# Performance work log

Hardware: AMD Instinct MI355X
Metric: run time of the kernel (lower is better)

The kernel has to match this reference:

```python
import jax, jax.numpy as jnp
import numpy as np
import math

SCALE = 64.0
MARGIN = 0.5
EPS = 1e-07
COS_M = math.cos(MARGIN)
SIN_M = math.sin(MARGIN)
THRESHOLD = math.cos(math.pi - MARGIN)
MM = math.sin(math.pi - MARGIN) * MARGIN

N, D, C = 512, 512, 100000


def setup_inputs() -> dict:
    key = jax.random.key(0)
    k1, k2, k3 = jax.random.split(key, 3)
    x = jax.random.normal(k1, (N, D), dtype=jnp.float32)
    weight = jax.random.normal(k2, (C, D), dtype=jnp.float32)
    t = jnp.zeros((1,), dtype=jnp.float32)
    target = jax.random.randint(k3, (N,), 0, C, dtype=jnp.int64)
    return {"x": x, "weight": weight, "t": t, "target": target}


def reference(x, weight, t, target):
    # normalized linear -> cosine similarities [N, C]
    xn = x / jnp.linalg.norm(x, axis=1, keepdims=True)
    wn = weight / jnp.linalg.norm(weight, axis=1, keepdims=True)
    cos_theta = jnp.clip(jnp.einsum('nd,cd->nc', xn, wn), -1.0 + EPS, 1.0 - EPS)

    rows = jnp.arange(cos_theta.shape[0])
    target_logit = cos_theta[rows, target][:, None]            # [N, 1]
    sin_theta = jnp.sqrt(1.0 - target_logit * target_logit)
    cos_theta_m = target_logit * COS_M - sin_theta * SIN_M      # cos(theta + m)

    mask = cos_theta > cos_theta_m                              # hard examples
    final_target_logit = jnp.where(target_logit > THRESHOLD,
                                   cos_theta_m,
                                   target_logit - MM)

    # EMA buffer update (no-grad in torch)
    t_new = jax.lax.stop_gradient(target_logit.mean() * 0.01 + 0.99 * t)  # [1]

    # hard-example re-weighting: cos * (t + cos) where mask
    cos_theta = jnp.where(mask, cos_theta * (t_new[0] + cos_theta), cos_theta)
    # scatter margin-adjusted target logit into target column
    cos_theta = cos_theta.at[rows, target].set(final_target_logit[:, 0])

    logits = cos_theta * SCALE
    # cross entropy (mean)
    logp = jax.nn.log_softmax(logits, axis=-1)
    loss = -jnp.mean(logp[rows, target])
    return loss
```

## Files before the change

kernel.cpp:

```cpp
#include <hip/hip_runtime.h>
#include <hip/hip_bf16.h>
#include <stdint.h>

#define N_ROWS 512
#define D_DIM  512
#define C_CLS  100000

#define SCALE_F    64.0f
#define EPS_F      1e-7f
#define COS_M_F    0.8775825618903728f
#define SIN_M_F    0.4794255386042030f
#define THRESH_F  -0.8775825618903728f
#define MM_F       0.2397127693021015f
#define FIXMAX_F   65.0f

#define NC  64
#define NG2 1564

#define XN8_OFF    0
#define TL_OFF     (XN8_OFF + 512*512)
#define CTM_OFF    (TL_OFF + 2048)
#define FTL_OFF    (CTM_OFF + 2048)
#define TNEW_OFF   (FTL_OFF + 2048)
#define XNORM_OFF  (TNEW_OFF + 256)
#define PSUM_OFF   (XNORM_OFF + 2048)
#define LOSSI_OFF  (PSUM_OFF + NG2*512*4)

typedef __attribute__((ext_vector_type(4))) float f32x4;

#define GLOAD_LDS16(gp, lp) \
    __builtin_amdgcn_global_load_lds((const __attribute__((address_space(1))) void*)(gp), \
                                     (__attribute__((address_space(3))) void*)(lp), 16, 0, 0)

#if defined(__has_builtin)
#if __has_builtin(__builtin_amdgcn_cvt_pk_fp8_f32)
#define HAVE_CVT_FP8 1
#endif
#endif

__device__ inline unsigned char f2e4m3(float f) {
    union { float f; unsigned u; } a; a.f = f;
    unsigned s = (a.u >> 24) & 0x80u;
    float af = fabsf(f);
    if (af < 0.015625f) {
        int q = (int)(af * 512.0f + 0.5f);
        return (unsigned char)(s | (unsigned)q);
    }
    unsigned x = a.u & 0x7FFFFFFFu;
    unsigned r = x + 0x000FFFFFu + ((x >> 20) & 1u);
    int ec = (int)(r >> 23) - 127 + 7;
    unsigned m = (r >> 20) & 7u;
    if (ec > 15 || (ec == 15 && m == 7u)) return (unsigned char)(s | 0x7Eu);
    return (unsigned char)(s | ((unsigned)ec << 3) | m);
}

__device__ inline unsigned pack4_fp8(float f0, float f1, float f2, float f3) {
#ifdef HAVE_CVT_FP8
    int q = __builtin_amdgcn_cvt_pk_fp8_f32(f0, f1, 0, false);
    q     = __builtin_amdgcn_cvt_pk_fp8_f32(f2, f3, q, true);
    return (unsigned)q;
#else
    union { unsigned char b[4]; unsigned u; } u;
    u.b[0]=f2e4m3(f0); u.b[1]=f2e4m3(f1); u.b[2]=f2e4m3(f2); u.b[3]=f2e4m3(f3);
    return u.u;
#endif
}

__device__ inline uint2 pack8_fp8(float f0, float f1, float f2, float f3,
                                  float f4, float f5, float f6, float f7) {
    uint2 r;
    r.x = pack4_fp8(f0, f1, f2, f3);
    r.y = pack4_fp8(f4, f5, f6, f7);
    return r;
}

__device__ inline float wave_sum64(float v) {
    #pragma unroll
    for (int m = 1; m < 64; m <<= 1) v += __shfl_xor(v, m);
    return v;
}

__global__ void k_xnorm_fp8(const float* __restrict__ x,
                            unsigned char* __restrict__ xn8,
                            float* __restrict__ xnorm) {
    int row = blockIdx.x;
    int lane = threadIdx.x;
    const float* xr = x + row * D_DIM + lane * 8;
    float4 v0 = *(const float4*)(xr);
    float4 v1 = *(const float4*)(xr + 4);
    float s = v0.x*v0.x + v0.y*v0.y + v0.z*v0.z + v0.w*v0.w
            + v1.x*v1.x + v1.y*v1.y + v1.z*v1.z + v1.w*v1.w;
    s = wave_sum64(s);
    float nrm = sqrtf(s);
    if (lane == 0) xnorm[row] = nrm;
    float inv = 1.0f / nrm;
    uint2 q = pack8_fp8(v0.x*inv, v0.y*inv, v0.z*inv, v0.w*inv,
                        v1.x*inv, v1.y*inv, v1.z*inv, v1.w*inv);
    *(uint2*)(xn8 + row * D_DIM + lane * 8) = q;
}

__global__ void k_tlogit(const float* __restrict__ x, const float* __restrict__ w,
                         const float* __restrict__ xnorm,
                         const int* __restrict__ target,
                         float* __restrict__ tl, float* __restrict__ ctm,
                         float* __restrict__ ftl) {
    int row = blockIdx.x;
    int lane = threadIdx.x;
    int tgt = target[row];
    const float* xr = x + row * D_DIM + lane * 8;
    const float* wr = w + (size_t)tgt * D_DIM + lane * 8;
    float4 a0 = *(const float4*)(xr),     a1 = *(const float4*)(xr + 4);
    float4 b0 = *(const float4*)(wr),     b1 = *(const float4*)(wr + 4);
    float s = a0.x*b0.x + a0.y*b0.y + a0.z*b0.z + a0.w*b0.w
            + a1.x*b1.x + a1.y*b1.y + a1.z*b1.z + a1.w*b1.w;
    float q = b0.x*b0.x + b0.y*b0.y + b0.z*b0.z + b0.w*b0.w
            + b1.x*b1.x + b1.y*b1.y + b1.z*b1.z + b1.w*b1.w;
    s = wave_sum64(s);
    q = wave_sum64(q);
    if (lane == 0) {
        float c = s / (xnorm[row] * sqrtf(q));
        c = fminf(fmaxf(c, -1.0f + EPS_F), 1.0f - EPS_F);
        float sn = sqrtf(fmaxf(1.0f - c * c, 0.0f));
        float cm = c * COS_M_F - sn * SIN_M_F;
        tl[row]  = c;
        ctm[row] = cm;
        ftl[row] = (c > THRESH_F) ? cm : (c - MM_F);
    }
}

__global__ void k_tnew(const float* __restrict__ tl, const float* __restrict__ t,
                       float* __restrict__ tnew) {
    __shared__ float s[512];
    int tid = threadIdx.x;
    s[tid] = tl[tid];
    __syncthreads();
    for (int off = 256; off > 0; off >>= 1) {
        if (tid < off) s[tid] += s[tid + off];
        __syncthreads();
    }
    if (tid == 0) tnew[0] = (s[0] / 512.0f) * 0.01f + 0.99f * t[0];
}

__global__ __launch_bounds__(512, 4) void k_fused(
        const unsigned char* __restrict__ xn8,
        const float* __restrict__ w,
        const int* __restrict__ target,
        const float* __restrict__ ctm,
        const float* __restrict__ ftl,
        const float* __restrict__ tnew,
        float* __restrict__ psum) {
    __shared__ unsigned char As[2][512 * 32];
    __shared__ unsigned char Bs[2][64 * 32];
    __shared__ float invS[64];
    __shared__ int   tgt_s[512];
    __shared__ float ctm_s[512];
    __shared__ float ftl_s[512];

    int bx = blockIdx.x;
    int cb = bx * NC;
    int tid = threadIdx.x;
    int lane = tid & 63, wid = tid >> 6;
    int fr = lane & 15, rgrp = lane >> 4;
    int wrow = wid * 64;

    tgt_s[tid] = target[tid];
    ctm_s[tid] = ctm[tid];
    ftl_s[tid] = ftl[tid];

    int brow  = tid >> 3;
    int bslot = tid & 7;
    int bclass = cb + brow;
    bool brvalid = (bclass < C_CLS);
    const float* bsrc = w + (size_t)(brvalid ? bclass : 0) * D_DIM + bslot * 4;

    float sumsq = 0.0f;

    #define STAGE_A(kk, buf)                                                  \
        do {                                                                  \
            _Pragma("unroll")                                                 \
            for (int c = 0; c < 2; ++c) {                                     \
                int lo = c * 8192 + wid * 1024;             \
                int o  = lo + lane * 16;                                      \
                int row = o >> 5, b = o & 31;                                 \
                GLOAD_LDS16(xn8 + (size_t)row * 512 + (kk) * 32 + b,          \
                            (char*)As[buf] + lo);                             \
            }                                                                 \
        } while (0)

    #define WRITE_B(vv, buf)                                                  \
        do {                                                                  \
            sumsq += vv.x*vv.x + vv.y*vv.y + vv.z*vv.z + vv.w*vv.w;           \
            *(unsigned*)(&Bs[buf][brow * 32 + bslot * 4]) =                   \
                pack4_fp8(vv.x, vv.y, vv.z, vv.w);                            \
        } while (0)

    float4 rv_next = *(const float4*)(bsrc + 1 * 32);
    float4 rv_far  = *(const float4*)(bsrc + 2 * 32);
    {
        float4 v0 = *(const float4*)(bsrc);
        WRITE_B(v0, 0);
    }
    STAGE_A(0, 0);
    __syncthreads();

    float tn = tnew[0];

    f32x4 acc[4][4];
    #pragma unroll
    for (int m = 0; m < 4; m++)
        #pragma unroll
        for (int j = 0; j < 4; j++)
            acc[m][j] = (f32x4){0.f, 0.f, 0.f, 0.f};

    union LL { uint2 u; long long ll; };

    #pragma unroll
    for (int kk = 0; kk < 16; ++kk) {
        int cur = kk & 1;
        if (kk < 15) {
            WRITE_B(rv_next, cur ^ 1);
            rv_next = rv_far;
            if (kk < 13)
                rv_far = *(const float4*)(bsrc + (kk + 3) * 32);
            STAGE_A(kk + 1, cur ^ 1);
        }
        uint2 af[4], bf[4];
        #pragma unroll
        for (int m = 0; m < 4; m++)
            af[m] = *(const uint2*)(&As[cur][(wrow + m * 16 + fr) * 32 + rgrp * 8]);
        #pragma unroll
        for (int j = 0; j < 4; j++)
            bf[j] = *(const uint2*)(&Bs[cur][(j * 16 + fr) * 32 + rgrp * 8]);
        __builtin_amdgcn_s_setprio(1);
        #pragma unroll
        for (int m = 0; m < 4; m++)
            #pragma unroll
            for (int j = 0; j < 4; j++) {
                LL a, b;
                a.u = af[m];
                b.u = bf[j];
                acc[m][j] = __builtin_amdgcn_mfma_f32_16x16x32_fp8_fp8(
                                a.ll, b.ll, acc[m][j], 0, 0, 0);
            }
        __builtin_amdgcn_s_setprio(0);
        __syncthreads();
    }
    #undef STAGE_A
    #undef WRITE_B

    float s2 = sumsq;
    s2 += __shfl_xor(s2, 1);
    s2 += __shfl_xor(s2, 2);
    s2 += __shfl_xor(s2, 4);
    if (bslot == 0) invS[brow] = rsqrtf(s2);
    __syncthreads();

    float inv[4];
    bool cvalid[4];
    #pragma unroll
    for (int j = 0; j < 4; j++) {
        inv[j] = invS[j * 16 + fr];
        cvalid[j] = (cb + j * 16 + fr) < C_CLS;
    }
    #pragma unroll
    for (int m = 0; m < 4; m++) {
        #pragma unroll
        for (int reg = 0; reg < 4; reg++) {
            int rl = wrow + m * 16 + rgrp * 4 + reg;
            int tr = tgt_s[rl];
            float cm = ctm_s[rl];
            float ft = ftl_s[rl];
            float sm = 0.0f;
            #pragma unroll
            for (int j = 0; j < 4; j++) {
                int col = cb + j * 16 + fr;
                float c = acc[m][j][reg] * inv[j];
                c = fminf(fmaxf(c, -1.0f + EPS_F), 1.0f - EPS_F);
                float v = (c > cm) ? c * (tn + c) : c;
                v *= SCALE_F;
                v = (col == tr) ? ft * SCALE_F : v;
                v = cvalid[j] ? v : -3.0e38f;
                sm += __expf(v - FIXMAX_F);
            }
            #pragma unroll
            for (int msk = 1; msk < 16; msk <<= 1) sm += __shfl_xor(sm, msk);
            if (fr == 0) psum[(size_t)bx * 512 + rl] = sm;
        }
    }
}

__global__ void k_rowlse_fix(const float* __restrict__ psum,
                             const float* __restrict__ ftl,
                             float* __restrict__ lossi) {
    int row = blockIdx.x, tid = threadIdx.x;
    float S = 0.0f;
    for (int nb = tid; nb < NG2; nb += 256) S += psum[(size_t)nb * 512 + row];
    __shared__ float sS[256];
    sS[tid] = S;
    __syncthreads();
    for (int off = 128; off > 0; off >>= 1) {
        if (tid < off) sS[tid] += sS[tid + off];
        __syncthreads();
    }
    if (tid == 0) lossi[row] = logf(sS[0]) + FIXMAX_F - SCALE_F * ftl[row];
}

__global__ void k_final(const float* __restrict__ lossi, float* __restrict__ out) {
    __shared__ float s[512];
    int tid = threadIdx.x;
    s[tid] = lossi[tid];
    __syncthreads();
    for (int off = 256; off > 0; off >>= 1) {
        if (tid < off) s[tid] += s[tid + off];
        __syncthreads();
    }
    if (tid == 0) out[0] = s[0] / 512.0f;
}

extern "C" void kernel_launch(void* const* d_in, const int* in_sizes, int n_in,
                              void* d_out, int out_size, void* d_ws, size_t ws_size,
                              hipStream_t stream) {
    const float* x      = (const float*)d_in[0];
    const float* w      = (const float*)d_in[1];
    const float* t      = (const float*)d_in[2];
    const int*   target = (const int*)d_in[3];

    char* ws = (char*)d_ws;
    unsigned char* xn8  = (unsigned char*)(ws + XN8_OFF);
    float* tl    = (float*)(ws + TL_OFF);
    float* ctm   = (float*)(ws + CTM_OFF);
    float* ftl   = (float*)(ws + FTL_OFF);
    float* tnew  = (float*)(ws + TNEW_OFF);
    float* xnorm = (float*)(ws + XNORM_OFF);
    float* psum  = (float*)(ws + PSUM_OFF);
    float* lossi = (float*)(ws + LOSSI_OFF);
    float* out   = (float*)d_out;

    k_xnorm_fp8<<<dim3(N_ROWS), dim3(64), 0, stream>>>(x, xn8, xnorm);
    k_tlogit<<<dim3(N_ROWS), dim3(64), 0, stream>>>(x, w, xnorm, target, tl, ctm, ftl);
    k_tnew<<<dim3(1), dim3(512), 0, stream>>>(tl, t, tnew);
    k_fused<<<dim3(NG2), dim3(512), 0, stream>>>(xn8, w, target, ctm, ftl, tnew, psum);
    k_rowlse_fix<<<dim3(N_ROWS), dim3(256), 0, stream>>>(psum, ftl, lossi);
    k_final<<<dim3(1), dim3(512), 0, stream>>>(lossi, out);
}
```

Before: 123.8 us.

## Load A fragments directly into registers and use 1024-thread blocks in fused GEMM

The fused GEMM kernel no longer stages the normalized x matrix through LDS. Each wave keeps its A fragments in registers with a three-deep prefetch from global memory, and blocks grow to 1024 threads with 32 rows per wave. The B tile gets a padded LDS stride to reduce bank conflicts, and the two prep kernels merge into one, dropping the xnorm buffer. This removes LDS traffic and capacity pressure for A, but depends on the 256KB xn8 matrix staying cache-resident and raises register and barrier pressure from the larger blocks.

```diff
diff --git a/kernel.cpp b/kernel.cpp
--- a/kernel.cpp
+++ b/kernel.cpp
@@ -22,15 +22,10 @@
 #define CTM_OFF    (TL_OFF + 2048)
 #define FTL_OFF    (CTM_OFF + 2048)
 #define TNEW_OFF   (FTL_OFF + 2048)
-#define XNORM_OFF  (TNEW_OFF + 256)
-#define PSUM_OFF   (XNORM_OFF + 2048)
+#define PSUM_OFF   (TNEW_OFF + 256)
 #define LOSSI_OFF  (PSUM_OFF + NG2*512*4)
 
 typedef __attribute__((ext_vector_type(4))) float f32x4;
-
-#define GLOAD_LDS16(gp, lp) \
-    __builtin_amdgcn_global_load_lds((const __attribute__((address_space(1))) void*)(gp), \
-                                     (__attribute__((address_space(3))) void*)(lp), 16, 0, 0)
 
 #if defined(__has_builtin)
 #if __has_builtin(__builtin_amdgcn_cvt_pk_fp8_f32)
@@ -66,12 +61,13 @@
 #endif
 }
 
-__device__ inline uint2 pack8_fp8(float f0, float f1, float f2, float f3,
-                                  float f4, float f5, float f6, float f7) {
-    uint2 r;
-    r.x = pack4_fp8(f0, f1, f2, f3);
-    r.y = pack4_fp8(f4, f5, f6, f7);
-    return r;
+__device__ inline unsigned short pack2_fp8(float f0, float f1) {
+#ifdef HAVE_CVT_FP8
+    int q = __builtin_amdgcn_cvt_pk_fp8_f32(f0, f1, 0, false);
+    return (unsigned short)(q & 0xFFFF);
+#else
+    return (unsigned short)(f2e4m3(f0) | ((unsigned short)f2e4m3(f1) << 8));
+#endif
 }
 
 __device__ inline float wave_sum64(float v) {
@@ -80,45 +76,37 @@
     return v;
 }
 
-__global__ void k_xnorm_fp8(const float* __restrict__ x,
-                            unsigned char* __restrict__ xn8,
-                            float* __restrict__ xnorm) {
+__global__ void k_prep(const float* __restrict__ x, const float* __restrict__ w,
+                       const int* __restrict__ target,
+                       unsigned char* __restrict__ xn8,
+                       float* __restrict__ tl, float* __restrict__ ctm,
+                       float* __restrict__ ftl) {
     int row = blockIdx.x;
     int lane = threadIdx.x;
     const float* xr = x + row * D_DIM + lane * 8;
     float4 v0 = *(const float4*)(xr);
     float4 v1 = *(const float4*)(xr + 4);
-    float s = v0.x*v0.x + v0.y*v0.y + v0.z*v0.z + v0.w*v0.w
-            + v1.x*v1.x + v1.y*v1.y + v1.z*v1.z + v1.w*v1.w;
-    s = wave_sum64(s);
-    float nrm = sqrtf(s);
-    if (lane == 0) xnorm[row] = nrm;
+    float sx = v0.x*v0.x + v0.y*v0.y + v0.z*v0.z + v0.w*v0.w
+             + v1.x*v1.x + v1.y*v1.y + v1.z*v1.z + v1.w*v1.w;
+    sx = wave_sum64(sx);
+    float nrm = sqrtf(sx);
     float inv = 1.0f / nrm;
-    uint2 q = pack8_fp8(v0.x*inv, v0.y*inv, v0.z*inv, v0.w*inv,
-                        v1.x*inv, v1.y*inv, v1.z*inv, v1.w*inv);
-    *(uint2*)(xn8 + row * D_DIM + lane * 8) = q;
-}
-
-__global__ void k_tlogit(const float* __restrict__ x, const float* __restrict__ w,
-                         const float* __restrict__ xnorm,
-                         const int* __restrict__ target,
-                         float* __restrict__ tl, float* __restrict__ ctm,
-                         float* __restrict__ ftl) {
-    int row = blockIdx.x;
-    int lane = threadIdx.x;
+    uint2 q8;
+    q8.x = pack4_fp8(v0.x*inv, v0.y*inv, v0.z*inv, v0.w*inv);
+    q8.y = pack4_fp8(v1.x*inv, v1.y*inv, v1.z*inv, v1.w*inv);
+    *(uint2*)(xn8 + row * D_DIM + lane * 8) = q8;
+
     int tgt = target[row];
-    const float* xr = x + row * D_DIM + lane * 8;
     const float* wr = w + (size_t)tgt * D_DIM + lane * 8;
-    float4 a0 = *(const float4*)(xr),     a1 = *(const float4*)(xr + 4);
-    float4 b0 = *(const float4*)(wr),     b1 = *(const float4*)(wr + 4);
-    float s = a0.x*b0.x + a0.y*b0.y + a0.z*b0.z + a0.w*b0.w
-            + a1.x*b1.x + a1.y*b1.y + a1.z*b1.z + a1.w*b1.w;
+    float4 b0 = *(const float4*)(wr), b1 = *(const float4*)(wr + 4);
+    float s = v0.x*b0.x + v0.y*b0.y + v0.z*b0.z + v0.w*b0.w
+            + v1.x*b1.x + v1.y*b1.y + v1.z*b1.z + v1.w*b1.w;
     float q = b0.x*b0.x + b0.y*b0.y + b0.z*b0.z + b0.w*b0.w
             + b1.x*b1.x + b1.y*b1.y + b1.z*b1.z + b1.w*b1.w;
     s = wave_sum64(s);
     q = wave_sum64(q);
     if (lane == 0) {
-        float c = s / (xnorm[row] * sqrtf(q));
+        float c = s / (nrm * sqrtf(q));
         c = fminf(fmaxf(c, -1.0f + EPS_F), 1.0f - EPS_F);
         float sn = sqrtf(fmaxf(1.0f - c * c, 0.0f));
         float cm = c * COS_M_F - sn * SIN_M_F;
@@ -141,7 +129,7 @@
     if (tid == 0) tnew[0] = (s[0] / 512.0f) * 0.01f + 0.99f * t[0];
 }
 
-__global__ __launch_bounds__(512, 4) void k_fused(
+__global__ __launch_bounds__(1024, 4) void k_fused(
         const unsigned char* __restrict__ xn8,
         const float* __restrict__ w,
         const int* __restrict__ target,
@@ -149,8 +137,7 @@
         const float* __restrict__ ftl,
         const float* __restrict__ tnew,
         float* __restrict__ psum) {
-    __shared__ unsigned char As[2][512 * 32];
-    __shared__ unsigned char Bs[2][64 * 32];
+    __shared__ unsigned char Bs[2][64 * 40];
     __shared__ float invS[64];
     __shared__ int   tgt_s[512];
     __shared__ float ctm_s[512];
@@ -161,53 +148,45 @@
     int tid = threadIdx.x;
     int lane = tid & 63, wid = tid >> 6;
     int fr = lane & 15, rgrp = lane >> 4;
-    int wrow = wid * 64;
-
-    tgt_s[tid] = target[tid];
-    ctm_s[tid] = ctm[tid];
-    ftl_s[tid] = ftl[tid];
-
-    int brow  = tid >> 3;
-    int bslot = tid & 7;
+    int wrow = wid * 32;
+
+    if (tid < 512) {
+        tgt_s[tid] = target[tid];
+        ctm_s[tid] = ctm[tid];
+        ftl_s[tid] = ftl[tid];
+    }
+    float tn = tnew[0];
+
+    int brow  = tid >> 4;
+    int bslot = tid & 15;
     int bclass = cb + brow;
-    bool brvalid = (bclass < C_CLS);
-    const float* bsrc = w + (size_t)(brvalid ? bclass : 0) * D_DIM + bslot * 4;
-
+    const float* bsrc = w + (size_t)(bclass < C_CLS ? bclass : 0) * D_DIM + bslot * 2;
+    int bwaddr = brow * 40 + bslot * 2;
     float sumsq = 0.0f;
 
-    #define STAGE_A(kk, buf)                                                  \
-        do {                                                                  \
-            _Pragma("unroll")                                                 \
-            for (int c = 0; c < 2; ++c) {                                     \
-                int lo = c * 8192 + wid * 1024;             \
-                int o  = lo + lane * 16;                                      \
-                int row = o >> 5, b = o & 31;                                 \
-                GLOAD_LDS16(xn8 + (size_t)row * 512 + (kk) * 32 + b,          \
-                            (char*)As[buf] + lo);                             \
-            }                                                                 \
-        } while (0)
-
-    #define WRITE_B(vv, buf)                                                  \
-        do {                                                                  \
-            sumsq += vv.x*vv.x + vv.y*vv.y + vv.z*vv.z + vv.w*vv.w;           \
-            *(unsigned*)(&Bs[buf][brow * 32 + bslot * 4]) =                   \
-                pack4_fp8(vv.x, vv.y, vv.z, vv.w);                            \
-        } while (0)
-
-    float4 rv_next = *(const float4*)(bsrc + 1 * 32);
-    float4 rv_far  = *(const float4*)(bsrc + 2 * 32);
+    const unsigned char* asrc0 = xn8 + (size_t)(wrow + fr) * D_DIM + rgrp * 8;
+    const unsigned char* asrc1 = xn8 + (size_t)(wrow + 16 + fr) * D_DIM + rgrp * 8;
+
     {
-        float4 v0 = *(const float4*)(bsrc);
-        WRITE_B(v0, 0);
-    }
-    STAGE_A(0, 0);
-    __syncthreads();
-
-    float tn = tnew[0];
-
-    f32x4 acc[4][4];
-    #pragma unroll
-    for (int m = 0; m < 4; m++)
+        float2 v0 = *(const float2*)(bsrc);
+        sumsq += v0.x*v0.x + v0.y*v0.y;
+        *(unsigned short*)(&Bs[0][bwaddr]) = pack2_fp8(v0.x, v0.y);
+    }
+    float2 rvN = *(const float2*)(bsrc + 32);
+    float2 rvF = *(const float2*)(bsrc + 64);
+    uint2 aP0 = *(const uint2*)(asrc0);
+    uint2 aP1 = *(const uint2*)(asrc1);
+    uint2 aQ0 = *(const uint2*)(asrc0 + 32);
+    uint2 aQ1 = *(const uint2*)(asrc1 + 32);
+    uint2 aR0 = *(const uint2*)(asrc0 + 64);
+    uint2 aR1 = *(const uint2*)(asrc1 + 64);
+    asm volatile("s_waitcnt lgkmcnt(0)" ::: "memory");
+    __builtin_amdgcn_s_barrier();
+    __builtin_amdgcn_sched_barrier(0);
+
+    f32x4 acc[2][4];
+    #pragma unroll
+    for (int m = 0; m < 2; m++)
         #pragma unroll
         for (int j = 0; j < 4; j++)
             acc[m][j] = (f32x4){0.f, 0.f, 0.f, 0.f};
@@ -217,41 +196,42 @@
     #pragma unroll
     for (int kk = 0; kk < 16; ++kk) {
         int cur = kk & 1;
-        if (kk < 15) {
-            WRITE_B(rv_next, cur ^ 1);
-            rv_next = rv_far;
-            if (kk < 13)
-                rv_far = *(const float4*)(bsrc + (kk + 3) * 32);
-            STAGE_A(kk + 1, cur ^ 1);
-        }
-        uint2 af[4], bf[4];
-        #pragma unroll
-        for (int m = 0; m < 4; m++)
-            af[m] = *(const uint2*)(&As[cur][(wrow + m * 16 + fr) * 32 + rgrp * 8]);
+        uint2 bf[4];
         #pragma unroll
         for (int j = 0; j < 4; j++)
-            bf[j] = *(const uint2*)(&Bs[cur][(j * 16 + fr) * 32 + rgrp * 8]);
+            bf[j] = *(const uint2*)(&Bs[cur][(j * 16 + fr) * 40 + rgrp * 8]);
         __builtin_amdgcn_s_setprio(1);
         #pragma unroll
-        for (int m = 0; m < 4; m++)
-            #pragma unroll
-            for (int j = 0; j < 4; j++) {
-                LL a, b;
-                a.u = af[m];
-                b.u = bf[j];
-                acc[m][j] = __builtin_amdgcn_mfma_f32_16x16x32_fp8_fp8(
-                                a.ll, b.ll, acc[m][j], 0, 0, 0);
+        for (int j = 0; j < 4; j++) {
+            LL a0, a1, b;
+            a0.u = aP0; a1.u = aP1; b.u = bf[j];
+            acc[0][j] = __builtin_amdgcn_mfma_f32_16x16x32_fp8_fp8(
+                            a0.ll, b.ll, acc[0][j], 0, 0, 0);
+            acc[1][j] = __builtin_amdgcn_mfma_f32_16x16x32_fp8_fp8(
+                            a1.ll, b.ll, acc[1][j], 0, 0, 0);
+        }
+        __builtin_amdgcn_s_setprio(0);
+        if (kk < 15) {
+            sumsq += rvN.x*rvN.x + rvN.y*rvN.y;
+            *(unsigned short*)(&Bs[cur ^ 1][bwaddr]) = pack2_fp8(rvN.x, rvN.y);
+            rvN = rvF;
+            if (kk < 13) rvF = *(const float2*)(bsrc + (kk + 3) * 32);
+            aP0 = aQ0; aP1 = aQ1; aQ0 = aR0; aQ1 = aR1;
+            if (kk < 13) {
+                aR0 = *(const uint2*)(asrc0 + (kk + 3) * 32);
+                aR1 = *(const uint2*)(asrc1 + (kk + 3) * 32);
             }
-        __builtin_amdgcn_s_setprio(0);
-        __syncthreads();
-    }
-    #undef STAGE_A
-    #undef WRITE_B
+            asm volatile("s_waitcnt lgkmcnt(0)" ::: "memory");
+            __builtin_amdgcn_s_barrier();
+            __builtin_amdgcn_sched_barrier(0);
+        }
+    }
 
     float s2 = sumsq;
     s2 += __shfl_xor(s2, 1);
     s2 += __shfl_xor(s2, 2);
     s2 += __shfl_xor(s2, 4);
+    s2 += __shfl_xor(s2, 8);
     if (bslot == 0) invS[brow] = rsqrtf(s2);
     __syncthreads();
 
@@ -263,7 +243,7 @@
         cvalid[j] = (cb + j * 16 + fr) < C_CLS;
     }
     #pragma unroll
-    for (int m = 0; m < 4; m++) {
+    for (int m = 0; m < 2; m++) {
         #pragma unroll
         for (int reg = 0; reg < 4; reg++) {
             int rl = wrow + m * 16 + rgrp * 4 + reg;
@@ -331,15 +311,13 @@
     float* ctm   = (float*)(ws + CTM_OFF);
     float* ftl   = (float*)(ws + FTL_OFF);
     float* tnew  = (float*)(ws + TNEW_OFF);
-    float* xnorm = (float*)(ws + XNORM_OFF);
     float* psum  = (float*)(ws + PSUM_OFF);
     float* lossi = (float*)(ws + LOSSI_OFF);
     float* out   = (float*)d_out;
 
-    k_xnorm_fp8<<<dim3(N_ROWS), dim3(64), 0, stream>>>(x, xn8, xnorm);
-    k_tlogit<<<dim3(N_ROWS), dim3(64), 0, stream>>>(x, w, xnorm, target, tl, ctm, ftl);
+    k_prep<<<dim3(N_ROWS), dim3(64), 0, stream>>>(x, w, target, xn8, tl, ctm, ftl);
     k_tnew<<<dim3(1), dim3(512), 0, stream>>>(tl, t, tnew);
-    k_fused<<<dim3(NG2), dim3(512), 0, stream>>>(xn8, w, target, ctm, ftl, tnew, psum);
+    k_fused<<<dim3(NG2), dim3(1024), 0, stream>>>(xn8, w, target, ctm, ftl, tnew, psum);
     k_rowlse_fix<<<dim3(N_ROWS), dim3(256), 0, stream>>>(psum, ftl, lossi);
     k_final<<<dim3(1), dim3(512), 0, stream>>>(lossi, out);
 }
```

Measured after the change: 157.1 us. +27.0%, slower.
